# Kernel tuning notes

Measured on AMD Instinct MI355X. Metric: run time of the kernel, lower is better.

## Reference

```python
import jax, jax.numpy as jnp
import numpy as np

N_NODES = 50000
N_EDGES = 800000
FIN = 128
FQK = 128
FV = 128
H = 8


def setup_inputs() -> dict:
    key = jax.random.key(0)
    k1, k2, k3, k4, k5 = jax.random.split(key, 5)
    x = jax.random.normal(k1, (N_NODES, FIN), dtype=jnp.float32)
    # nn.Linear(Fin, 2*Fqk+Fv, bias=False): weight shape [Ftot, Fin]
    W = jax.random.normal(k2, (2 * FQK + FV, FIN), dtype=jnp.float32) / np.sqrt(FIN)
    # src must be sorted (scatter_* assume batch[-1]+1 segments)
    src = jnp.sort(jax.random.randint(k3, (N_EDGES,), 0, N_NODES))
    dest = jax.random.randint(k4, (N_EDGES,), 0, N_NODES)
    ei = jnp.stack([src, dest])
    batch = jnp.sort(jax.random.randint(k5, (N_NODES,), 0, 64))
    return {"x": x, "W": W, "batch": batch, "ei": ei}


def reference(x, W, batch, ei):
    n = x.shape[0]
    Fh = FQK // H    # 16
    Fhv = FV // H    # 16
    scaling = float(Fh) ** (-0.5)
    src, dest = ei[0], ei[1]

    qkv = x @ W.T                                   # [n, 2*Fqk+Fv]
    q = (qkv[:, :FQK] * scaling).reshape(n, H, Fh)
    k = qkv[:, FQK:2 * FQK].reshape(n, H, Fh)
    v = qkv[:, 2 * FQK:].reshape(n, H, Fhv)

    # per-edge attention scores, one per head: [E, H]
    aw = jnp.einsum('ehf,ehf->eh', q[src], k[dest])
    # faithful to original scatter_softmax: subtract GLOBAL per-head max
    aw = aw - aw.max(axis=0)
    ex = jnp.exp(aw)
    denom = jax.ops.segment_sum(ex, src, num_segments=n)[src]   # [E, H]
    a = ex / denom

    out = jax.ops.segment_sum(a[:, :, None] * v[dest], src, num_segments=n)  # [n, H, Fhv]
    return out.reshape(n, H * Fhv)
```

## Files before the change

### kernel.cpp

```cpp
#include <hip/hip_runtime.h>
#include <hip/hip_bf16.h>
#include <math.h>

#define FIN_ 128
#define FQK_ 128

typedef __attribute__((ext_vector_type(8))) short short8v;
typedef __attribute__((ext_vector_type(4))) float float4v;

__device__ __forceinline__ unsigned short f2bf(float f) {
    unsigned u = __float_as_uint(f);
    u += 0x7fffu + ((u >> 16) & 1u);
    return (unsigned short)(u >> 16);
}

__device__ __forceinline__ short8v pack8(float4 a, float4 b) {
    short8v r;
    r[0] = (short)f2bf(a.x); r[1] = (short)f2bf(a.y);
    r[2] = (short)f2bf(a.z); r[3] = (short)f2bf(a.w);
    r[4] = (short)f2bf(b.x); r[5] = (short)f2bf(b.y);
    r[6] = (short)f2bf(b.z); r[7] = (short)f2bf(b.w);
    return r;
}

__global__ __launch_bounds__(256) void gemm_qkv_mfma(const float* __restrict__ x,
                                                     const float* __restrict__ W,
                                                     float* __restrict__ qbuf,
                                                     unsigned short* __restrict__ kv,
                                                     int n) {
    __shared__ unsigned short xs[128][68];
    __shared__ unsigned short ws[128][68];
    const int row0 = blockIdx.x * 128;
    const int col0 = blockIdx.y * 128;
    const int t = threadIdx.x;
    const int lane = t & 63;
    const int wave = t >> 6;
    const int wr = wave >> 1, wc = wave & 1;
    const int l15 = lane & 15, kg = lane >> 4;

    float4v acc[4][4];
#pragma unroll
    for (int i = 0; i < 4; ++i)
#pragma unroll
        for (int j = 0; j < 4; ++j) acc[i][j] = (float4v)0.f;

    const int r5 = t >> 3;
    const int c8 = (t & 7) * 8;

    for (int half = 0; half < 2; ++half) {
        __syncthreads();
#pragma unroll
        for (int p = 0; p < 4; ++p) {
            const int row = p * 32 + r5;
            const int gxr = row0 + row;
            float4 u0, u1;
            if (gxr < n) {
                u0 = *(const float4*)&x[(size_t)gxr * FIN_ + half * 64 + c8];
                u1 = *(const float4*)&x[(size_t)gxr * FIN_ + half * 64 + c8 + 4];
            } else {
                u0 = make_float4(0.f, 0.f, 0.f, 0.f); u1 = u0;
            }
            *(short8v*)&xs[row][c8] = pack8(u0, u1);
            const float4 w0 = *(const float4*)&W[(size_t)(col0 + row) * FIN_ + half * 64 + c8];
            const float4 w1 = *(const float4*)&W[(size_t)(col0 + row) * FIN_ + half * 64 + c8 + 4];
            *(short8v*)&ws[row][c8] = pack8(w0, w1);
        }
        __syncthreads();
#pragma unroll
        for (int ks = 0; ks < 2; ++ks) {
            const int kcol = ks * 32 + kg * 8;
            short8v a[4], b[4];
#pragma unroll
            for (int mi = 0; mi < 4; ++mi)
                a[mi] = *(short8v*)&xs[wr * 64 + mi * 16 + l15][kcol];
#pragma unroll
            for (int ni = 0; ni < 4; ++ni)
                b[ni] = *(short8v*)&ws[wc * 64 + ni * 16 + l15][kcol];
#pragma unroll
            for (int mi = 0; mi < 4; ++mi)
#pragma unroll
                for (int ni = 0; ni < 4; ++ni)
                    acc[mi][ni] = __builtin_amdgcn_mfma_f32_16x16x32_bf16(
                        a[mi], b[ni], acc[mi][ni], 0, 0, 0);
        }
    }

    const int orow = kg * 4;
#pragma unroll
    for (int mi = 0; mi < 4; ++mi) {
#pragma unroll
        for (int reg = 0; reg < 4; ++reg) {
            const int r = row0 + wr * 64 + mi * 16 + orow + reg;
            if (r >= n) continue;
#pragma unroll
            for (int ni = 0; ni < 4; ++ni) {
                const int c = wc * 64 + ni * 16 + l15;
                const float v = acc[mi][ni][reg];
                if (col0 == 0) {
                    qbuf[(size_t)r * FIN_ + c] = v * 0.25f;
                } else {
                    const int base = (col0 == 128) ? 0 : 128;
                    kv[(size_t)r * 256 + base + c] = f2bf(v);
                }
            }
        }
    }
}

__global__ void build_rowptr(const int* __restrict__ src, int nE,
                             int* __restrict__ rowptr, int n) {
    int i = blockIdx.x * blockDim.x + threadIdx.x;
    if (i > n) return;
    int lo = 0, hi = nE;
    while (lo < hi) {
        int mid = (lo + hi) >> 1;
        if (src[mid] < i) lo = mid + 1; else hi = mid;
    }
    rowptr[i] = lo;
}

#define LOF(w) __uint_as_float((w) << 16)
#define HIF(w) __uint_as_float((w) & 0xffff0000u)

__global__ __launch_bounds__(256) void attn_edges_ep(const float* __restrict__ qbuf,
                                                     const unsigned short* __restrict__ kv,
                                                     const int* __restrict__ rowptr,
                                                     const int* __restrict__ dest,
                                                     float* __restrict__ out, int n) {
    const int wave = threadIdx.x >> 6;
    const int node = blockIdx.x * 4 + wave;
    if (node >= n) return;
    const int lane = threadIdx.x & 63;
    const int j = lane >> 3;
    const int h = lane & 7;
    const int ppos = ((j & 1) << 3) | ((j & 2) << 1) | ((j & 4) >> 1);
    float* outp = &out[(size_t)node * FIN_ + h * 16 + ppos];

    const int e0 = rowptr[node];
    const int e1 = rowptr[node + 1];
    if (e0 == e1) {
        *(float2*)outp = make_float2(0.f, 0.f);
        return;
    }

    float qa[16];
    {
        const float4* qp = (const float4*)&qbuf[(size_t)node * FIN_ + h * 16];
        float4 a = qp[0], b = qp[1], c = qp[2], d = qp[3];
        qa[0]=a.x; qa[1]=a.y; qa[2]=a.z; qa[3]=a.w;
        qa[4]=b.x; qa[5]=b.y; qa[6]=b.z; qa[7]=b.w;
        qa[8]=c.x; qa[9]=c.y; qa[10]=c.z; qa[11]=c.w;
        qa[12]=d.x; qa[13]=d.y; qa[14]=d.z; qa[15]=d.w;
    }

    float lsum = 0.f;
    float acc[16];
#pragma unroll
    for (int i = 0; i < 16; ++i) acc[i] = 0.f;

    const int hoff = h << 4;
    for (int eb = e0; eb < e1; eb += 8) {
        const int my_e = eb + j;
        const bool valid = my_e < e1;
        const int ee = valid ? my_e : (e1 - 1);
        const unsigned d = (unsigned)dest[ee];
        const unsigned off = (d << 8) + hoff;
        const uint4 k0 = *(const uint4*)(kv + off);
        const uint4 k1 = *(const uint4*)(kv + off + 8);
        const uint4 v0 = *(const uint4*)(kv + off + 128);
        const uint4 v1 = *(const uint4*)(kv + off + 136);

        float s;
        s  = qa[0]  * LOF(k0.x) + qa[1]  * HIF(k0.x);
        s += qa[2]  * LOF(k0.y) + qa[3]  * HIF(k0.y);
        s += qa[4]  * LOF(k0.z) + qa[5]  * HIF(k0.z);
        s += qa[6]  * LOF(k0.w) + qa[7]  * HIF(k0.w);
        s += qa[8]  * LOF(k1.x) + qa[9]  * HIF(k1.x);
        s += qa[10] * LOF(k1.y) + qa[11] * HIF(k1.y);
        s += qa[12] * LOF(k1.z) + qa[13] * HIF(k1.z);
        s += qa[14] * LOF(k1.w) + qa[15] * HIF(k1.w);

        const float p = valid ? __expf(s) : 0.f;
        lsum += p;
        acc[0]  += p * LOF(v0.x); acc[1]  += p * HIF(v0.x);
        acc[2]  += p * LOF(v0.y); acc[3]  += p * HIF(v0.y);
        acc[4]  += p * LOF(v0.z); acc[5]  += p * HIF(v0.z);
        acc[6]  += p * LOF(v0.w); acc[7]  += p * HIF(v0.w);
        acc[8]  += p * LOF(v1.x); acc[9]  += p * HIF(v1.x);
        acc[10] += p * LOF(v1.y); acc[11] += p * HIF(v1.y);
        acc[12] += p * LOF(v1.z); acc[13] += p * HIF(v1.z);
        acc[14] += p * LOF(v1.w); acc[15] += p * HIF(v1.w);
    }

    lsum += __shfl_xor(lsum, 8);
    lsum += __shfl_xor(lsum, 16);
    lsum += __shfl_xor(lsum, 32);

    float r8[8];
    {
        const bool b = (j & 1) != 0;
#pragma unroll
        for (int i = 0; i < 8; ++i) {
            const float keep = b ? acc[i + 8] : acc[i];
            const float send = b ? acc[i] : acc[i + 8];
            r8[i] = keep + __shfl_xor(send, 8);
        }
    }
    float r4[4];
    {
        const bool b = (j & 2) != 0;
#pragma unroll
        for (int i = 0; i < 4; ++i) {
            const float keep = b ? r8[i + 4] : r8[i];
            const float send = b ? r8[i] : r8[i + 4];
            r4[i] = keep + __shfl_xor(send, 16);
        }
    }
    float r2[2];
    {
        const bool b = (j & 4) != 0;
#pragma unroll
        for (int i = 0; i < 2; ++i) {
            const float keep = b ? r4[i + 2] : r4[i];
            const float send = b ? r4[i] : r4[i + 2];
            r2[i] = keep + __shfl_xor(send, 32);
        }
    }

    const float inv = (lsum > 0.f) ? 1.f / lsum : 0.f;
    *(float2*)outp = make_float2(r2[0] * inv, r2[1] * inv);
}

extern "C" void kernel_launch(void* const* d_in, const int* in_sizes, int n_in,
                              void* d_out, int out_size, void* d_ws, size_t ws_size,
                              hipStream_t stream) {
    const float* x = (const float*)d_in[0];
    const float* W = (const float*)d_in[1];
    const int* ei = (const int*)d_in[3];

    const int n = in_sizes[0] / FIN_;
    const int nE = in_sizes[3] / 2;
    const int* src = ei;
    const int* dest = ei + nE;

    float* qbuf = (float*)d_ws;
    unsigned short* kv = (unsigned short*)((char*)d_ws + (size_t)n * FIN_ * sizeof(float));
    int* rowptr = (int*)((char*)kv + (size_t)n * 256 * sizeof(unsigned short));
    float* out = (float*)d_out;

    build_rowptr<<<(n + 1 + 255) / 256, 256, 0, stream>>>(src, nE, rowptr, n);

    dim3 g1((n + 127) / 128, 3);
    gemm_qkv_mfma<<<g1, 256, 0, stream>>>(x, W, qbuf, kv, n);

    attn_edges_ep<<<(n + 3) / 4, 256, 0, stream>>>(qbuf, kv, rowptr, dest, out, n);
}
```

Baseline: 95.60 us.

## Pre-convert inputs to bf16, store q as bf16, unroll edge loop by two

A separate kernel now converts x and W to bf16 once, so the GEMM no longer rereads and converts fp32 x in each of its three column blocks. The q projection is stored as bf16 instead of fp32, which halves its footprint and its read in the attention kernel. The edge loop handles two edges per lane per iteration so more gathers are in flight at once. This adds a kernel launch plus an extra write and read of the bf16 x copy, and rounding q to bf16 slightly reduces precision.

New measurement: 94.65 us. About the same (-1.0%).

```diff
diff --git a/kernel.cpp b/kernel.cpp
--- a/kernel.cpp
+++ b/kernel.cpp
@@ -14,18 +14,34 @@
     return (unsigned short)(u >> 16);
 }
 
-__device__ __forceinline__ short8v pack8(float4 a, float4 b) {
+__global__ __launch_bounds__(256) void cvt_bf16(const float* __restrict__ x,
+                                                const float* __restrict__ W,
+                                                unsigned short* __restrict__ xb,
+                                                unsigned short* __restrict__ wb,
+                                                int nx8, int nw8) {
+    int i = blockIdx.x * blockDim.x + threadIdx.x;
+    const float* s;
+    unsigned short* d;
+    if (i < nx8) {
+        s = x + (size_t)i * 8; d = xb + (size_t)i * 8;
+    } else {
+        i -= nx8;
+        if (i >= nw8) return;
+        s = W + (size_t)i * 8; d = wb + (size_t)i * 8;
+    }
+    const float4 a = *(const float4*)s;
+    const float4 b = *(const float4*)(s + 4);
     short8v r;
     r[0] = (short)f2bf(a.x); r[1] = (short)f2bf(a.y);
     r[2] = (short)f2bf(a.z); r[3] = (short)f2bf(a.w);
     r[4] = (short)f2bf(b.x); r[5] = (short)f2bf(b.y);
     r[6] = (short)f2bf(b.z); r[7] = (short)f2bf(b.w);
-    return r;
-}
-
-__global__ __launch_bounds__(256) void gemm_qkv_mfma(const float* __restrict__ x,
-                                                     const float* __restrict__ W,
-                                                     float* __restrict__ qbuf,
+    *(short8v*)d = r;
+}
+
+__global__ __launch_bounds__(256) void gemm_qkv_mfma(const unsigned short* __restrict__ xb,
+                                                     const unsigned short* __restrict__ wb,
+                                                     unsigned short* __restrict__ qb,
                                                      unsigned short* __restrict__ kv,
                                                      int n) {
     __shared__ unsigned short xs[128][68];
@@ -53,17 +69,11 @@
         for (int p = 0; p < 4; ++p) {
             const int row = p * 32 + r5;
             const int gxr = row0 + row;
-            float4 u0, u1;
-            if (gxr < n) {
-                u0 = *(const float4*)&x[(size_t)gxr * FIN_ + half * 64 + c8];
-                u1 = *(const float4*)&x[(size_t)gxr * FIN_ + half * 64 + c8 + 4];
-            } else {
-                u0 = make_float4(0.f, 0.f, 0.f, 0.f); u1 = u0;
-            }
-            *(short8v*)&xs[row][c8] = pack8(u0, u1);
-            const float4 w0 = *(const float4*)&W[(size_t)(col0 + row) * FIN_ + half * 64 + c8];
-            const float4 w1 = *(const float4*)&W[(size_t)(col0 + row) * FIN_ + half * 64 + c8 + 4];
-            *(short8v*)&ws[row][c8] = pack8(w0, w1);
+            short8v vx = (short8v)0;
+            if (gxr < n) vx = *(const short8v*)(xb + (size_t)gxr * FIN_ + half * 64 + c8);
+            *(short8v*)&xs[row][c8] = vx;
+            *(short8v*)&ws[row][c8] =
+                *(const short8v*)(wb + (size_t)(col0 + row) * FIN_ + half * 64 + c8);
         }
         __syncthreads();
 #pragma unroll
@@ -97,7 +107,7 @@
                 const int c = wc * 64 + ni * 16 + l15;
                 const float v = acc[mi][ni][reg];
                 if (col0 == 0) {
-                    qbuf[(size_t)r * FIN_ + c] = v * 0.25f;
+                    qb[(size_t)r * FIN_ + c] = f2bf(v * 0.25f);
                 } else {
                     const int base = (col0 == 128) ? 0 : 128;
                     kv[(size_t)r * 256 + base + c] = f2bf(v);
@@ -122,7 +132,7 @@
 #define LOF(w) __uint_as_float((w) << 16)
 #define HIF(w) __uint_as_float((w) & 0xffff0000u)
 
-__global__ __launch_bounds__(256) void attn_edges_ep(const float* __restrict__ qbuf,
+__global__ __launch_bounds__(256) void attn_edges_ep(const unsigned short* __restrict__ qb,
                                                      const unsigned short* __restrict__ kv,
                                                      const int* __restrict__ rowptr,
                                                      const int* __restrict__ dest,
@@ -145,12 +155,12 @@
 
     float qa[16];
     {
-        const float4* qp = (const float4*)&qbuf[(size_t)node * FIN_ + h * 16];
-        float4 a = qp[0], b = qp[1], c = qp[2], d = qp[3];
-        qa[0]=a.x; qa[1]=a.y; qa[2]=a.z; qa[3]=a.w;
-        qa[4]=b.x; qa[5]=b.y; qa[6]=b.z; qa[7]=b.w;
-        qa[8]=c.x; qa[9]=c.y; qa[10]=c.z; qa[11]=c.w;
-        qa[12]=d.x; qa[13]=d.y; qa[14]=d.z; qa[15]=d.w;
+        const uint4 q0 = *(const uint4*)(qb + (size_t)node * FIN_ + h * 16);
+        const uint4 q1 = *(const uint4*)(qb + (size_t)node * FIN_ + h * 16 + 8);
+        qa[0]=LOF(q0.x); qa[1]=HIF(q0.x); qa[2]=LOF(q0.y); qa[3]=HIF(q0.y);
+        qa[4]=LOF(q0.z); qa[5]=HIF(q0.z); qa[6]=LOF(q0.w); qa[7]=HIF(q0.w);
+        qa[8]=LOF(q1.x); qa[9]=HIF(q1.x); qa[10]=LOF(q1.y); qa[11]=HIF(q1.y);
+        qa[12]=LOF(q1.z); qa[13]=HIF(q1.z); qa[14]=LOF(q1.w); qa[15]=HIF(q1.w);
     }
 
     float lsum = 0.f;
@@ -159,37 +169,62 @@
     for (int i = 0; i < 16; ++i) acc[i] = 0.f;
 
     const int hoff = h << 4;
-    for (int eb = e0; eb < e1; eb += 8) {
-        const int my_e = eb + j;
-        const bool valid = my_e < e1;
-        const int ee = valid ? my_e : (e1 - 1);
-        const unsigned d = (unsigned)dest[ee];
-        const unsigned off = (d << 8) + hoff;
-        const uint4 k0 = *(const uint4*)(kv + off);
-        const uint4 k1 = *(const uint4*)(kv + off + 8);
-        const uint4 v0 = *(const uint4*)(kv + off + 128);
-        const uint4 v1 = *(const uint4*)(kv + off + 136);
-
-        float s;
-        s  = qa[0]  * LOF(k0.x) + qa[1]  * HIF(k0.x);
-        s += qa[2]  * LOF(k0.y) + qa[3]  * HIF(k0.y);
-        s += qa[4]  * LOF(k0.z) + qa[5]  * HIF(k0.z);
-        s += qa[6]  * LOF(k0.w) + qa[7]  * HIF(k0.w);
-        s += qa[8]  * LOF(k1.x) + qa[9]  * HIF(k1.x);
-        s += qa[10] * LOF(k1.y) + qa[11] * HIF(k1.y);
-        s += qa[12] * LOF(k1.z) + qa[13] * HIF(k1.z);
-        s += qa[14] * LOF(k1.w) + qa[15] * HIF(k1.w);
-
-        const float p = valid ? __expf(s) : 0.f;
-        lsum += p;
-        acc[0]  += p * LOF(v0.x); acc[1]  += p * HIF(v0.x);
-        acc[2]  += p * LOF(v0.y); acc[3]  += p * HIF(v0.y);
-        acc[4]  += p * LOF(v0.z); acc[5]  += p * HIF(v0.z);
-        acc[6]  += p * LOF(v0.w); acc[7]  += p * HIF(v0.w);
-        acc[8]  += p * LOF(v1.x); acc[9]  += p * HIF(v1.x);
-        acc[10] += p * LOF(v1.y); acc[11] += p * HIF(v1.y);
-        acc[12] += p * LOF(v1.z); acc[13] += p * HIF(v1.z);
-        acc[14] += p * LOF(v1.w); acc[15] += p * HIF(v1.w);
+    for (int eb = e0; eb < e1; eb += 16) {
+        const int eA = eb + j;
+        const int eB = eb + 8 + j;
+        const bool vA = eA < e1;
+        const bool vB = eB < e1;
+        const unsigned dA = (unsigned)dest[vA ? eA : (e1 - 1)];
+        const unsigned dB = (unsigned)dest[vB ? eB : (e1 - 1)];
+        const unsigned offA = (dA << 8) + hoff;
+        const unsigned offB = (dB << 8) + hoff;
+        const uint4 k0A = *(const uint4*)(kv + offA);
+        const uint4 k1A = *(const uint4*)(kv + offA + 8);
+        const uint4 v0A = *(const uint4*)(kv + offA + 128);
+        const uint4 v1A = *(const uint4*)(kv + offA + 136);
+        const uint4 k0B = *(const uint4*)(kv + offB);
+        const uint4 k1B = *(const uint4*)(kv + offB + 8);
+        const uint4 v0B = *(const uint4*)(kv + offB + 128);
+        const uint4 v1B = *(const uint4*)(kv + offB + 136);
+
+        float sA;
+        sA  = qa[0]  * LOF(k0A.x) + qa[1]  * HIF(k0A.x);
+        sA += qa[2]  * LOF(k0A.y) + qa[3]  * HIF(k0A.y);
+        sA += qa[4]  * LOF(k0A.z) + qa[5]  * HIF(k0A.z);
+        sA += qa[6]  * LOF(k0A.w) + qa[7]  * HIF(k0A.w);
+        sA += qa[8]  * LOF(k1A.x) + qa[9]  * HIF(k1A.x);
+        sA += qa[10] * LOF(k1A.y) + qa[11] * HIF(k1A.y);
+        sA += qa[12] * LOF(k1A.z) + qa[13] * HIF(k1A.z);
+        sA += qa[14] * LOF(k1A.w) + qa[15] * HIF(k1A.w);
+        float sB;
+        sB  = qa[0]  * LOF(k0B.x) + qa[1]  * HIF(k0B.x);
+        sB += qa[2]  * LOF(k0B.y) + qa[3]  * HIF(k0B.y);
+        sB += qa[4]  * LOF(k0B.z) + qa[5]  * HIF(k0B.z);
+        sB += qa[6]  * LOF(k0B.w) + qa[7]  * HIF(k0B.w);
+        sB += qa[8]  * LOF(k1B.x) + qa[9]  * HIF(k1B.x);
+        sB += qa[10] * LOF(k1B.y) + qa[11] * HIF(k1B.y);
+        sB += qa[12] * LOF(k1B.z) + qa[13] * HIF(k1B.z);
+        sB += qa[14] * LOF(k1B.w) + qa[15] * HIF(k1B.w);
+
+        const float pA = vA ? __expf(sA) : 0.f;
+        const float pB = vB ? __expf(sB) : 0.f;
+        lsum += pA + pB;
+        acc[0]  += pA * LOF(v0A.x) + pB * LOF(v0B.x);
+        acc[1]  += pA * HIF(v0A.x) + pB * HIF(v0B.x);
+        acc[2]  += pA * LOF(v0A.y) + pB * LOF(v0B.y);
+        acc[3]  += pA * HIF(v0A.y) + pB * HIF(v0B.y);
+        acc[4]  += pA * LOF(v0A.z) + pB * LOF(v0B.z);
+        acc[5]  += pA * HIF(v0A.z) + pB * HIF(v0B.z);
+        acc[6]  += pA * LOF(v0A.w) + pB * LOF(v0B.w);
+        acc[7]  += pA * HIF(v0A.w) + pB * HIF(v0B.w);
+        acc[8]  += pA * LOF(v1A.x) + pB * LOF(v1B.x);
+        acc[9]  += pA * HIF(v1A.x) + pB * HIF(v1B.x);
+        acc[10] += pA * LOF(v1A.y) + pB * LOF(v1B.y);
+        acc[11] += pA * HIF(v1A.y) + pB * HIF(v1B.y);
+        acc[12] += pA * LOF(v1A.z) + pB * LOF(v1B.z);
+        acc[13] += pA * HIF(v1A.z) + pB * HIF(v1B.z);
+        acc[14] += pA * LOF(v1A.w) + pB * LOF(v1B.w);
+        acc[15] += pA * HIF(v1A.w) + pB * HIF(v1B.w);
     }
 
     lsum += __shfl_xor(lsum, 8);
@@ -239,19 +274,26 @@
     const int* ei = (const int*)d_in[3];
 
     const int n = in_sizes[0] / FIN_;
+    const int nW = in_sizes[1];
     const int nE = in_sizes[3] / 2;
     const int* src = ei;
     const int* dest = ei + nE;
 
-    float* qbuf = (float*)d_ws;
-    unsigned short* kv = (unsigned short*)((char*)d_ws + (size_t)n * FIN_ * sizeof(float));
-    int* rowptr = (int*)((char*)kv + (size_t)n * 256 * sizeof(unsigned short));
+    char* w = (char*)d_ws;
+    unsigned short* qb = (unsigned short*)w;        w += (size_t)n * FIN_ * 2;
+    unsigned short* kv = (unsigned short*)w;        w += (size_t)n * 256 * 2;
+    int* rowptr = (int*)w;                          w += ((size_t)(n + 1) * 4 + 15) & ~(size_t)15;
+    unsigned short* xb = (unsigned short*)w;        w += (size_t)n * FIN_ * 2;
+    unsigned short* wb = (unsigned short*)w;
     float* out = (float*)d_out;
 
+    const int nx8 = n * FIN_ / 8, nw8 = nW / 8;
+    cvt_bf16<<<(nx8 + nw8 + 255) / 256, 256, 0, stream>>>(x, W, xb, wb, nx8, nw8);
+
     build_rowptr<<<(n + 1 + 255) / 256, 256, 0, stream>>>(src, nE, rowptr, n);
 
     dim3 g1((n + 127) / 128, 3);
-    gemm_qkv_mfma<<<g1, 256, 0, stream>>>(x, W, qbuf, kv, n);
-
-    attn_edges_ep<<<(n + 3) / 4, 256, 0, stream>>>(qbuf, kv, rowptr, dest, out, n);
-}
+    gemm_qkv_mfma<<<g1, 256, 0, stream>>>(xb, wb, qb, kv, n);
+
+    attn_edges_ep<<<(n + 3) / 4, 256, 0, stream>>>(qb, kv, rowptr, dest, out, n);
+}
```
